# Kernel tuning notes

Hardware: AMD Instinct MI355X
Metric: run time of the kernel (lower is better)

Reference implementation:

```python
import jax, jax.numpy as jnp
import numpy as np

VOCAB = 50000
EMBED = 256
LABELS = 2
DEPTH = 10          # complete binary tree: 2**DEPTH leaves
B = 256             # batch of trees
L = 2 ** DEPTH      # leaves per tree


def setup_inputs() -> dict:
    key = jax.random.key(0)
    ks = jax.random.split(key, 7)
    token_ids = jax.random.randint(ks[0], (B, L), 0, VOCAB)
    labels = jax.random.randint(ks[1], (B,), 0, LABELS)
    emb = jax.random.normal(ks[2], (VOCAB, EMBED), dtype=jnp.float32)
    W_w = jax.random.normal(ks[3], (EMBED, 2 * EMBED), dtype=jnp.float32) * (1.0 / np.sqrt(2 * EMBED))
    W_b = jax.random.normal(ks[4], (EMBED,), dtype=jnp.float32) * 0.01
    P_w = jax.random.normal(ks[5], (LABELS, EMBED), dtype=jnp.float32) * (1.0 / np.sqrt(EMBED))
    P_b = jax.random.normal(ks[6], (LABELS,), dtype=jnp.float32) * 0.01
    return {"token_ids": token_ids, "labels": labels, "emb": emb,
            "W_w": W_w, "W_b": W_b, "P_w": P_w, "P_b": P_b}


def reference(token_ids, labels, emb, W_w, W_b, P_w, P_b):
    # Leaves: relu(embedding(token))  -> [B, L, E]
    x = jax.nn.relu(emb[token_ids])
    # Level-by-level combine: currentNode = relu(W @ cat(left, right) + b)
    # Leaf order is left-to-right, so adjacent pairs (2k, 2k+1) are siblings;
    # reshape concatenates (left, right) along features, matching torch.cat((l, r), 1).
    while x.shape[1] > 1:
        bsz, n, e = x.shape
        lr = x.reshape(bsz, n // 2, 2 * e)                       # [B, n/2, 2E]
        x = jax.nn.relu(jnp.einsum('bnf,ef->bne', lr, W_w) + W_b)
    root = x[:, 0]                                               # [B, E]
    logits = root @ P_w.T + P_b                                  # [B, label_size]
    prediction = jnp.argmax(logits, axis=1)
    logp = jax.nn.log_softmax(logits, axis=-1)
    loss = -jnp.take_along_axis(logp, labels[:, None], axis=1)[:, 0]  # per-tree CE
    return prediction, loss
```

## Files before the change

### kernel.cpp

```cpp
#include <hip/hip_runtime.h>
#include <hip/hip_bf16.h>
#include <math.h>

#define EMBED   256
#define KDIM    512
#define BATCH   256
#define BM      128
#define VOCAB   50000

typedef float  f32x4   __attribute__((ext_vector_type(4)));
typedef __bf16 bf16x8  __attribute__((ext_vector_type(8)));
typedef unsigned short ushort8 __attribute__((ext_vector_type(8)));

__device__ __forceinline__ unsigned short f2h(float f) {
    unsigned int u = __float_as_uint(f);
    u += 0x7FFFu + ((u >> 16) & 1u);
    return (unsigned short)(u >> 16);
}
__device__ __forceinline__ float h2f(unsigned short h) {
    return __uint_as_float(((unsigned int)h) << 16);
}
__device__ __forceinline__ void gload16(const void* g, void* l) {
    __builtin_amdgcn_global_load_lds(
        (const __attribute__((address_space(1))) unsigned int*)g,
        (__attribute__((address_space(3))) unsigned int*)l, 16, 0, 0);
}

__global__ __launch_bounds__(256) void prep_emb(const float* __restrict__ emb,
                                                unsigned short* __restrict__ Eh,
                                                unsigned short* __restrict__ El)
{
    const size_t base = ((size_t)blockIdx.x * 256 + threadIdx.x) * 8;
    float v[8];
    *(float4*)&v[0] = *(const float4*)&emb[base];
    *(float4*)&v[4] = *(const float4*)&emb[base + 4];
    ushort8 hs, ls;
    #pragma unroll
    for (int i = 0; i < 8; ++i) {
        const float f = fmaxf(v[i], 0.f);
        const unsigned short h = f2h(f);
        hs[i] = h;
        ls[i] = f2h(f - h2f(h));
    }
    *(ushort8*)&Eh[base] = hs;
    *(ushort8*)&El[base] = ls;
}

__global__ __launch_bounds__(256) void prep_w(const float* __restrict__ W,
                                              unsigned short* __restrict__ Wh,
                                              unsigned short* __restrict__ Wl)
{
    const int i = blockIdx.x * 256 + threadIdx.x;
    const float w = W[i];
    const unsigned short h = f2h(w);
    Wh[i] = h;
    Wl[i] = f2h(w - h2f(h));
}

template<int LV1, int WPREP>
__global__ __launch_bounds__(512) void gemm_tree(
    const unsigned short* __restrict__ Xh, const unsigned short* __restrict__ Xl,
    const unsigned short* __restrict__ Wh, const unsigned short* __restrict__ Wl,
    const float*  __restrict__ Wf,
    const float*  __restrict__ bias,
    unsigned short* __restrict__ Yh, unsigned short* __restrict__ Yl,
    const int* __restrict__ tok,
    const unsigned short* __restrict__ Eh, const unsigned short* __restrict__ El)
{
    __shared__ __align__(16) unsigned short AhL[4096], AlL[4096];
    __shared__ __align__(16) unsigned short BhL[8192], BlL[8192];

    const int tid = threadIdx.x;
    const int wid = tid >> 6;
    const int l   = tid & 63;
    const int q   = l >> 4;
    const int rr  = l & 15;
    const int m0  = blockIdx.x * BM;

    const int waveM = wid >> 2;
    const int waveN = wid & 3;

    int tk0 = 0, tk1 = 0;
    if constexpr (LV1) {
        const int r = m0 + wid * 16 + rr;
        tk0 = tok[2 * r];
        tk1 = tok[2 * r + 1];
    }

    f32x4 acc[4][4] = {};

    for (int t = 0; t < 16; ++t) {
        const int k0   = t << 5;
        const int joff = k0 >> 8;
        const int c    = (k0 & 255) + q * 8;

        if constexpr (LV1) {
            const size_t off = (size_t)(joff ? tk1 : tk0) * EMBED + c;
            gload16(Eh + off, &AhL[wid * 512]);
            gload16(El + off, &AlL[wid * 512]);
        } else {
            const size_t off = (size_t)(2 * (m0 + wid * 16 + rr) + joff) * EMBED + c;
            gload16(Xh + off, &AhL[wid * 512]);
            gload16(Xl + off, &AlL[wid * 512]);
        }

        #pragma unroll
        for (int g = 0; g < 2; ++g) {
            const int s = wid + g * 8;
            if constexpr (WPREP) {
                const size_t off = (size_t)(s * 16 + rr) * KDIM + k0 + q * 8;
                gload16(Wh + off, &BhL[s * 512]);
                gload16(Wl + off, &BlL[s * 512]);
            } else {
                const float* ws = Wf + (size_t)(s * 16 + rr) * KDIM + k0 + q * 8;
                float v[8];
                *(float4*)&v[0] = *(const float4*)ws;
                *(float4*)&v[4] = *(const float4*)(ws + 4);
                ushort8 hs, ls;
                #pragma unroll
                for (int i = 0; i < 8; ++i) {
                    const unsigned short h = f2h(v[i]);
                    hs[i] = h;
                    ls[i] = f2h(v[i] - h2f(h));
                }
                *(ushort8*)&BhL[s * 512 + l * 8] = hs;
                *(ushort8*)&BlL[s * 512 + l * 8] = ls;
            }
        }

        __syncthreads();

        bf16x8 ah[4], al[4], bh[4], bl[4];
        #pragma unroll
        for (int mi = 0; mi < 4; ++mi) {
            ah[mi] = *(const bf16x8*)&AhL[(waveM * 4 + mi) * 512 + l * 8];
            al[mi] = *(const bf16x8*)&AlL[(waveM * 4 + mi) * 512 + l * 8];
        }
        #pragma unroll
        for (int ni = 0; ni < 4; ++ni) {
            bh[ni] = *(const bf16x8*)&BhL[(waveN * 4 + ni) * 512 + l * 8];
            bl[ni] = *(const bf16x8*)&BlL[(waveN * 4 + ni) * 512 + l * 8];
        }
        #pragma unroll
        for (int mi = 0; mi < 4; ++mi)
            #pragma unroll
            for (int ni = 0; ni < 4; ++ni)
                acc[mi][ni] = __builtin_amdgcn_mfma_f32_16x16x32_bf16(ah[mi], bh[ni], acc[mi][ni], 0, 0, 0);
        #pragma unroll
        for (int mi = 0; mi < 4; ++mi)
            #pragma unroll
            for (int ni = 0; ni < 4; ++ni)
                acc[mi][ni] = __builtin_amdgcn_mfma_f32_16x16x32_bf16(al[mi], bh[ni], acc[mi][ni], 0, 0, 0);
        #pragma unroll
        for (int mi = 0; mi < 4; ++mi)
            #pragma unroll
            for (int ni = 0; ni < 4; ++ni)
                acc[mi][ni] = __builtin_amdgcn_mfma_f32_16x16x32_bf16(ah[mi], bl[ni], acc[mi][ni], 0, 0, 0);

        __syncthreads();
    }

    #pragma unroll
    for (int ni = 0; ni < 4; ++ni) {
        const int col = waveN * 64 + ni * 16 + rr;
        const float bv = bias[col];
        #pragma unroll
        for (int mi = 0; mi < 4; ++mi) {
            const int row0 = m0 + waveM * 64 + mi * 16 + q * 4;
            #pragma unroll
            for (int jj = 0; jj < 4; ++jj) {
                const float y = fmaxf(acc[mi][ni][jj] + bv, 0.f);
                const unsigned short h = f2h(y);
                Yh[(size_t)(row0 + jj) * EMBED + col] = h;
                Yl[(size_t)(row0 + jj) * EMBED + col] = f2h(y - h2f(h));
            }
        }
    }
}

template<int WPREP>
__global__ __launch_bounds__(256) void tail_kernel(
    const unsigned short* __restrict__ A4h, const unsigned short* __restrict__ A4l,
    const unsigned short* __restrict__ Wh, const unsigned short* __restrict__ Wl,
    const float* __restrict__ Wf, const float* __restrict__ bias,
    const float* __restrict__ Pw, const float* __restrict__ Pb,
    const int* __restrict__ labels, float* __restrict__ out)
{
    __shared__ __align__(16) unsigned short X0h[8192], X0l[8192];
    __shared__ __align__(16) unsigned short X1h[4096], X1l[4096];
    __shared__ __align__(16) unsigned short BhT[2][8192], BlT[2][8192];
    __shared__ __align__(16) unsigned short Asth[2][1024], Astl[2][1024];

    const int tid = threadIdx.x;
    const int w   = tid >> 6;
    const int l   = tid & 63;
    const int q   = l >> 4;
    const int rr  = l & 15;
    const int b   = blockIdx.x;

    auto stageB = [&](int buf, int k0) {
        if constexpr (WPREP) {
            #pragma unroll
            for (int j = 0; j < 8; ++j) {
                const int sb = w * 8 + j;
                const int s  = sb & 15;
                const size_t off = (size_t)(s * 16 + rr) * KDIM + k0 + q * 8;
                if (sb < 16) gload16(Wh + off, &BhT[buf][s * 512]);
                else         gload16(Wl + off, &BlT[buf][s * 512]);
            }
        } else {
            #pragma unroll
            for (int j = 0; j < 4; ++j) {
                const int u = w * 4 + j;
                const float* ws = Wf + (size_t)(u * 16 + rr) * KDIM + k0 + q * 8;
                float v[8];
                *(float4*)&v[0] = *(const float4*)ws;
                *(float4*)&v[4] = *(const float4*)(ws + 4);
                ushort8 hs, ls;
                #pragma unroll
                for (int i = 0; i < 8; ++i) {
                    const unsigned short h = f2h(v[i]);
                    hs[i] = h;
                    ls[i] = f2h(v[i] - h2f(h));
                }
                *(ushort8*)&BhT[buf][u * 512 + l * 8] = hs;
                *(ushort8*)&BlT[buf][u * 512 + l * 8] = ls;
            }
        }
    };

    auto stageA = [&](int buf, int t) {
        if (w < 2) {
            const int k0   = t * 32;
            const int joff = k0 >> 8;
            const int c    = (k0 & 255) + q * 8;
            const size_t off = (size_t)(64 * b + 2 * (w * 16 + rr) + joff) * EMBED + c;
            gload16(A4h + off, &Asth[buf][w * 512]);
            gload16(A4l + off, &Astl[buf][w * 512]);
        }
    };

    float bv[4];
    #pragma unroll
    for (int ni = 0; ni < 4; ++ni) bv[ni] = bias[w * 64 + ni * 16 + rr];

    stageB(0, 0);
    stageA(0, 0);
    __syncthreads();

    int g = 0;
    for (int s = 0; s < 6; ++s) {
        unsigned short* srch = (s & 1) ? X0h : X1h;
        unsigned short* srcl = (s & 1) ? X0l : X1l;
        unsigned short* dsth = (s & 1) ? X1h : X0h;
        unsigned short* dstl = (s & 1) ? X1l : X0l;
        const int Mout = 32 >> s;

        f32x4 acc[2][4] = {};
        for (int t = 0; t < 16; ++t, ++g) {
            const int cur = g & 1;
            if (g < 95) stageB(cur ^ 1, ((t + 1) & 15) * 32);
            if (s == 0 && t < 15) stageA(cur ^ 1, t + 1);

            const int k0   = t * 32;
            const int joff = k0 >> 8;
            const int c    = (k0 & 255) + q * 8;

            bf16x8 a_h0, a_l0;
            if (s == 0) {
                a_h0 = *(const bf16x8*)&Asth[cur][l * 8];
                a_l0 = *(const bf16x8*)&Astl[cur][l * 8];
            } else {
                const int row = 2 * rr + joff;
                const int idx = (row * 256 + c) ^ ((row & 7) << 3);
                a_h0 = *(const bf16x8*)&srch[idx];
                a_l0 = *(const bf16x8*)&srcl[idx];
            }

            bf16x8 bh4[4], bl4[4];
            #pragma unroll
            for (int ni = 0; ni < 4; ++ni) {
                bh4[ni] = *(const bf16x8*)&BhT[cur][(w * 4 + ni) * 512 + l * 8];
                bl4[ni] = *(const bf16x8*)&BlT[cur][(w * 4 + ni) * 512 + l * 8];
            }
            #pragma unroll
            for (int ni = 0; ni < 4; ++ni)
                acc[0][ni] = __builtin_amdgcn_mfma_f32_16x16x32_bf16(a_h0, bh4[ni], acc[0][ni], 0, 0, 0);
            #pragma unroll
            for (int ni = 0; ni < 4; ++ni)
                acc[0][ni] = __builtin_amdgcn_mfma_f32_16x16x32_bf16(a_l0, bh4[ni], acc[0][ni], 0, 0, 0);
            #pragma unroll
            for (int ni = 0; ni < 4; ++ni)
                acc[0][ni] = __builtin_amdgcn_mfma_f32_16x16x32_bf16(a_h0, bl4[ni], acc[0][ni], 0, 0, 0);

            if (s == 0) {
                const bf16x8 a_h1 = *(const bf16x8*)&Asth[cur][512 + l * 8];
                const bf16x8 a_l1 = *(const bf16x8*)&Astl[cur][512 + l * 8];
                #pragma unroll
                for (int ni = 0; ni < 4; ++ni)
                    acc[1][ni] = __builtin_amdgcn_mfma_f32_16x16x32_bf16(a_h1, bh4[ni], acc[1][ni], 0, 0, 0);
                #pragma unroll
                for (int ni = 0; ni < 4; ++ni)
                    acc[1][ni] = __builtin_amdgcn_mfma_f32_16x16x32_bf16(a_l1, bh4[ni], acc[1][ni], 0, 0, 0);
                #pragma unroll
                for (int ni = 0; ni < 4; ++ni)
                    acc[1][ni] = __builtin_amdgcn_mfma_f32_16x16x32_bf16(a_h1, bl4[ni], acc[1][ni], 0, 0, 0);
            }
            __syncthreads();
        }

        #pragma unroll
        for (int ni = 0; ni < 4; ++ni) {
            const int col = w * 64 + ni * 16 + rr;
            #pragma unroll
            for (int jj = 0; jj < 4; ++jj) {
                const int row = q * 4 + jj;
                if (row < Mout) {
                    const float y = fmaxf(acc[0][ni][jj] + bv[ni], 0.f);
                    const unsigned short h = f2h(y);
                    const int idx = (row * 256 + col) ^ ((row & 7) << 3);
                    dsth[idx] = h;
                    dstl[idx] = f2h(y - h2f(h));
                }
            }
            if (s == 0) {
                #pragma unroll
                for (int jj = 0; jj < 4; ++jj) {
                    const int row = 16 + q * 4 + jj;
                    const float y = fmaxf(acc[1][ni][jj] + bv[ni], 0.f);
                    const unsigned short h = f2h(y);
                    const int idx = (row * 256 + col) ^ ((row & 7) << 3);
                    dsth[idx] = h;
                    dstl[idx] = f2h(y - h2f(h));
                }
            }
        }
        __syncthreads();
    }

    if (w == 0) {
        float s0 = 0.f, s1 = 0.f;
        #pragma unroll
        for (int i = 0; i < 4; ++i) {
            const int col = l + i * 64;
            const float x = h2f(X1h[col]) + h2f(X1l[col]);
            s0 = fmaf(x, Pw[col], s0);
            s1 = fmaf(x, Pw[EMBED + col], s1);
        }
        #pragma unroll
        for (int off = 32; off > 0; off >>= 1) {
            s0 += __shfl_down(s0, off);
            s1 += __shfl_down(s1, off);
        }
        if (l == 0) {
            const float l0 = s0 + Pb[0];
            const float l1 = s1 + Pb[1];
            const int pred = (l1 > l0) ? 1 : 0;
            const float m  = fmaxf(l0, l1);
            const float lse = m + logf(expf(l0 - m) + expf(l1 - m));
            const int lab = labels[b];
            out[b]         = (float)pred;
            out[BATCH + b] = lse - (lab ? l1 : l0);
        }
    }
}

extern "C" void kernel_launch(void* const* d_in, const int* in_sizes, int n_in,
                              void* d_out, int out_size, void* d_ws, size_t ws_size,
                              hipStream_t stream)
{
    const int*   token_ids = (const int*)d_in[0];
    const int*   labels    = (const int*)d_in[1];
    const float* emb       = (const float*)d_in[2];
    const float* W_w       = (const float*)d_in[3];
    const float* W_b       = (const float*)d_in[4];
    const float* P_w       = (const float*)d_in[5];
    const float* P_b       = (const float*)d_in[6];
    float*       out       = (float*)d_out;

    unsigned short* Ah_buf = (unsigned short*)d_ws;
    unsigned short* Al_buf = Ah_buf + (size_t)131072 * 256;
    unsigned short* Bh_buf = Al_buf + (size_t)131072 * 256;
    unsigned short* Bl_buf = Bh_buf + (size_t)65536 * 256;
    unsigned short* Wh     = Bl_buf + (size_t)65536 * 256;
    unsigned short* Wl     = Wh + 131072;
    unsigned short* Eh     = Bh_buf;
    unsigned short* El     = Bl_buf;

    const size_t need_wprep = ((size_t)131072 * 256 * 2 + (size_t)65536 * 256 * 2 + 2 * 131072) * 2;
    const bool wprep = ws_size >= need_wprep;

    if (wprep) prep_w<<<512, 256, 0, stream>>>(W_w, Wh, Wl);
    prep_emb<<<(VOCAB * EMBED) / 2048, 256, 0, stream>>>(emb, Eh, El);

    if (wprep) {
        gemm_tree<1,1><<<1024, 512, 0, stream>>>(nullptr, nullptr, Wh, Wl, W_w, W_b, Ah_buf, Al_buf, token_ids, Eh, El);
        gemm_tree<0,1><<< 512, 512, 0, stream>>>(Ah_buf, Al_buf, Wh, Wl, W_w, W_b, Bh_buf, Bl_buf, nullptr, nullptr, nullptr);
        gemm_tree<0,1><<< 256, 512, 0, stream>>>(Bh_buf, Bl_buf, Wh, Wl, W_w, W_b, Ah_buf, Al_buf, nullptr, nullptr, nullptr);
        gemm_tree<0,1><<< 128, 512, 0, stream>>>(Ah_buf, Al_buf, Wh, Wl, W_w, W_b, Bh_buf, Bl_buf, nullptr, nullptr, nullptr);
        tail_kernel<1><<<BATCH, 256, 0, stream>>>(Bh_buf, Bl_buf, Wh, Wl, W_w, W_b, P_w, P_b, labels, out);
    } else {
        gemm_tree<1,0><<<1024, 512, 0, stream>>>(nullptr, nullptr, Wh, Wl, W_w, W_b, Ah_buf, Al_buf, token_ids, Eh, El);
        gemm_tree<0,0><<< 512, 512, 0, stream>>>(Ah_buf, Al_buf, Wh, Wl, W_w, W_b, Bh_buf, Bl_buf, nullptr, nullptr, nullptr);
        gemm_tree<0,0><<< 256, 512, 0, stream>>>(Bh_buf, Bl_buf, Wh, Wl, W_w, W_b, Ah_buf, Al_buf, nullptr, nullptr, nullptr);
        gemm_tree<0,0><<< 128, 512, 0, stream>>>(Ah_buf, Al_buf, Wh, Wl, W_w, W_b, Bh_buf, Bl_buf, nullptr, nullptr, nullptr);
        tail_kernel<0><<<BATCH, 256, 0, stream>>>(Bh_buf, Bl_buf, Wh, Wl, W_w, W_b, P_w, P_b, labels, out);
    }
}
```

Before: 452.0 us.

## Split GEMM tree tiles along N and merge prep kernels into one launch

Each gemm_tree block now computes a 128x128 output tile with 256 threads instead of a 128x256 tile with 512 threads. The N dimension is split across a second grid axis, which doubles the block count and halves LDS use per block, so occupancy and parallelism should rise, especially on the small later levels. The cost is that each A tile (embedding gather or previous-level activations) is loaded twice, once per N half. The embedding and weight split-prep kernels are also fused into a single launch to save one kernel launch.

```diff
diff --git a/kernel.cpp b/kernel.cpp
--- a/kernel.cpp
+++ b/kernel.cpp
@@ -26,39 +26,41 @@
         (__attribute__((address_space(3))) unsigned int*)l, 16, 0, 0);
 }
 
-__global__ __launch_bounds__(256) void prep_emb(const float* __restrict__ emb,
+__global__ __launch_bounds__(256) void prep_all(const float* __restrict__ emb,
                                                 unsigned short* __restrict__ Eh,
-                                                unsigned short* __restrict__ El)
+                                                unsigned short* __restrict__ El,
+                                                const float* __restrict__ W,
+                                                unsigned short* __restrict__ Wh,
+                                                unsigned short* __restrict__ Wl,
+                                                int wprep)
 {
-    const size_t base = ((size_t)blockIdx.x * 256 + threadIdx.x) * 8;
-    float v[8];
-    *(float4*)&v[0] = *(const float4*)&emb[base];
-    *(float4*)&v[4] = *(const float4*)&emb[base + 4];
-    ushort8 hs, ls;
-    #pragma unroll
-    for (int i = 0; i < 8; ++i) {
-        const float f = fmaxf(v[i], 0.f);
-        const unsigned short h = f2h(f);
-        hs[i] = h;
-        ls[i] = f2h(f - h2f(h));
-    }
-    *(ushort8*)&Eh[base] = hs;
-    *(ushort8*)&El[base] = ls;
-}
-
-__global__ __launch_bounds__(256) void prep_w(const float* __restrict__ W,
-                                              unsigned short* __restrict__ Wh,
-                                              unsigned short* __restrict__ Wl)
-{
-    const int i = blockIdx.x * 256 + threadIdx.x;
-    const float w = W[i];
-    const unsigned short h = f2h(w);
-    Wh[i] = h;
-    Wl[i] = f2h(w - h2f(h));
+    const int bid = blockIdx.x;
+    if (bid < 6250) {
+        const size_t base = ((size_t)bid * 256 + threadIdx.x) * 8;
+        float v[8];
+        *(float4*)&v[0] = *(const float4*)&emb[base];
+        *(float4*)&v[4] = *(const float4*)&emb[base + 4];
+        ushort8 hs, ls;
+        #pragma unroll
+        for (int i = 0; i < 8; ++i) {
+            const float f = fmaxf(v[i], 0.f);
+            const unsigned short h = f2h(f);
+            hs[i] = h;
+            ls[i] = f2h(f - h2f(h));
+        }
+        *(ushort8*)&Eh[base] = hs;
+        *(ushort8*)&El[base] = ls;
+    } else if (wprep) {
+        const int i = (bid - 6250) * 256 + threadIdx.x;
+        const float w = W[i];
+        const unsigned short h = f2h(w);
+        Wh[i] = h;
+        Wl[i] = f2h(w - h2f(h));
+    }
 }
 
 template<int LV1, int WPREP>
-__global__ __launch_bounds__(512) void gemm_tree(
+__global__ __launch_bounds__(256) void gemm_tree(
     const unsigned short* __restrict__ Xh, const unsigned short* __restrict__ Xl,
     const unsigned short* __restrict__ Wh, const unsigned short* __restrict__ Wl,
     const float*  __restrict__ Wf,
@@ -68,23 +70,27 @@
     const unsigned short* __restrict__ Eh, const unsigned short* __restrict__ El)
 {
     __shared__ __align__(16) unsigned short AhL[4096], AlL[4096];
-    __shared__ __align__(16) unsigned short BhL[8192], BlL[8192];
+    __shared__ __align__(16) unsigned short BhL[4096], BlL[4096];
 
     const int tid = threadIdx.x;
-    const int wid = tid >> 6;
+    const int w   = tid >> 6;
     const int l   = tid & 63;
     const int q   = l >> 4;
     const int rr  = l & 15;
-    const int m0  = blockIdx.x * BM;
-
-    const int waveM = wid >> 2;
-    const int waveN = wid & 3;
-
-    int tk0 = 0, tk1 = 0;
+    const int m0  = blockIdx.y * BM;
+    const int n0  = blockIdx.x * 128;
+
+    const int waveM = w >> 1;
+    const int waveN = w & 1;
+
+    int tk[2][2];
     if constexpr (LV1) {
-        const int r = m0 + wid * 16 + rr;
-        tk0 = tok[2 * r];
-        tk1 = tok[2 * r + 1];
+        #pragma unroll
+        for (int g = 0; g < 2; ++g) {
+            const int r = m0 + (w + g * 4) * 16 + rr;
+            tk[g][0] = tok[2 * r];
+            tk[g][1] = tok[2 * r + 1];
+        }
     }
 
     f32x4 acc[4][4] = {};
@@ -94,25 +100,25 @@
         const int joff = k0 >> 8;
         const int c    = (k0 & 255) + q * 8;
 
-        if constexpr (LV1) {
-            const size_t off = (size_t)(joff ? tk1 : tk0) * EMBED + c;
-            gload16(Eh + off, &AhL[wid * 512]);
-            gload16(El + off, &AlL[wid * 512]);
-        } else {
-            const size_t off = (size_t)(2 * (m0 + wid * 16 + rr) + joff) * EMBED + c;
-            gload16(Xh + off, &AhL[wid * 512]);
-            gload16(Xl + off, &AlL[wid * 512]);
-        }
-
         #pragma unroll
         for (int g = 0; g < 2; ++g) {
-            const int s = wid + g * 8;
+            const int s = w + g * 4;
+            if constexpr (LV1) {
+                const int  tkg = joff ? tk[g][1] : tk[g][0];
+                const size_t off = (size_t)tkg * EMBED + c;
+                gload16(Eh + off, &AhL[s * 512]);
+                gload16(El + off, &AlL[s * 512]);
+            } else {
+                const size_t off = (size_t)(2 * (m0 + s * 16 + rr) + joff) * EMBED + c;
+                gload16(Xh + off, &AhL[s * 512]);
+                gload16(Xl + off, &AlL[s * 512]);
+            }
             if constexpr (WPREP) {
-                const size_t off = (size_t)(s * 16 + rr) * KDIM + k0 + q * 8;
-                gload16(Wh + off, &BhL[s * 512]);
-                gload16(Wl + off, &BlL[s * 512]);
+                const size_t woff = (size_t)(n0 + s * 16 + rr) * KDIM + k0 + q * 8;
+                gload16(Wh + woff, &BhL[s * 512]);
+                gload16(Wl + woff, &BlL[s * 512]);
             } else {
-                const float* ws = Wf + (size_t)(s * 16 + rr) * KDIM + k0 + q * 8;
+                const float* ws = Wf + (size_t)(n0 + s * 16 + rr) * KDIM + k0 + q * 8;
                 float v[8];
                 *(float4*)&v[0] = *(const float4*)ws;
                 *(float4*)&v[4] = *(const float4*)(ws + 4);
@@ -162,7 +168,7 @@
 
     #pragma unroll
     for (int ni = 0; ni < 4; ++ni) {
-        const int col = waveN * 64 + ni * 16 + rr;
+        const int col = n0 + waveN * 64 + ni * 16 + rr;
         const float bv = bias[col];
         #pragma unroll
         for (int mi = 0; mi < 4; ++mi) {
@@ -390,20 +396,19 @@
     const size_t need_wprep = ((size_t)131072 * 256 * 2 + (size_t)65536 * 256 * 2 + 2 * 131072) * 2;
     const bool wprep = ws_size >= need_wprep;
 
-    if (wprep) prep_w<<<512, 256, 0, stream>>>(W_w, Wh, Wl);
-    prep_emb<<<(VOCAB * EMBED) / 2048, 256, 0, stream>>>(emb, Eh, El);
+    prep_all<<<6762, 256, 0, stream>>>(emb, Eh, El, W_w, Wh, Wl, wprep ? 1 : 0);
 
     if (wprep) {
-        gemm_tree<1,1><<<1024, 512, 0, stream>>>(nullptr, nullptr, Wh, Wl, W_w, W_b, Ah_buf, Al_buf, token_ids, Eh, El);
-        gemm_tree<0,1><<< 512, 512, 0, stream>>>(Ah_buf, Al_buf, Wh, Wl, W_w, W_b, Bh_buf, Bl_buf, nullptr, nullptr, nullptr);
-        gemm_tree<0,1><<< 256, 512, 0, stream>>>(Bh_buf, Bl_buf, Wh, Wl, W_w, W_b, Ah_buf, Al_buf, nullptr, nullptr, nullptr);
-        gemm_tree<0,1><<< 128, 512, 0, stream>>>(Ah_buf, Al_buf, Wh, Wl, W_w, W_b, Bh_buf, Bl_buf, nullptr, nullptr, nullptr);
+        gemm_tree<1,1><<<dim3(2,1024), 256, 0, stream>>>(nullptr, nullptr, Wh, Wl, W_w, W_b, Ah_buf, Al_buf, token_ids, Eh, El);
+        gemm_tree<0,1><<<dim3(2, 512), 256, 0, stream>>>(Ah_buf, Al_buf, Wh, Wl, W_w, W_b, Bh_buf, Bl_buf, nullptr, nullptr, nullptr);
+        gemm_tree<0,1><<<dim3(2, 256), 256, 0, stream>>>(Bh_buf, Bl_buf, Wh, Wl, W_w, W_b, Ah_buf, Al_buf, nullptr, nullptr, nullptr);
+        gemm_tree<0,1><<<dim3(2, 128), 256, 0, stream>>>(Ah_buf, Al_buf, Wh, Wl, W_w, W_b, Bh_buf, Bl_buf, nullptr, nullptr, nullptr);
         tail_kernel<1><<<BATCH, 256, 0, stream>>>(Bh_buf, Bl_buf, Wh, Wl, W_w, W_b, P_w, P_b, labels, out);
     } else {
-        gemm_tree<1,0><<<1024, 512, 0, stream>>>(nullptr, nullptr, Wh, Wl, W_w, W_b, Ah_buf, Al_buf, token_ids, Eh, El);
-        gemm_tree<0,0><<< 512, 512, 0, stream>>>(Ah_buf, Al_buf, Wh, Wl, W_w, W_b, Bh_buf, Bl_buf, nullptr, nullptr, nullptr);
-        gemm_tree<0,0><<< 256, 512, 0, stream>>>(Bh_buf, Bl_buf, Wh, Wl, W_w, W_b, Ah_buf, Al_buf, nullptr, nullptr, nullptr);
-        gemm_tree<0,0><<< 128, 512, 0, stream>>>(Ah_buf, Al_buf, Wh, Wl, W_w, W_b, Bh_buf, Bl_buf, nullptr, nullptr, nullptr);
+        gemm_tree<1,0><<<dim3(2,1024), 256, 0, stream>>>(nullptr, nullptr, Wh, Wl, W_w, W_b, Ah_buf, Al_buf, token_ids, Eh, El);
+        gemm_tree<0,0><<<dim3(2, 512), 256, 0, stream>>>(Ah_buf, Al_buf, Wh, Wl, W_w, W_b, Bh_buf, Bl_buf, nullptr, nullptr, nullptr);
+        gemm_tree<0,0><<<dim3(2, 256), 256, 0, stream>>>(Bh_buf, Bl_buf, Wh, Wl, W_w, W_b, Ah_buf, Al_buf, nullptr, nullptr, nullptr);
+        gemm_tree<0,0><<<dim3(2, 128), 256, 0, stream>>>(Ah_buf, Al_buf, Wh, Wl, W_w, W_b, Bh_buf, Bl_buf, nullptr, nullptr, nullptr);
         tail_kernel<0><<<BATCH, 256, 0, stream>>>(Bh_buf, Bl_buf, Wh, Wl, W_w, W_b, P_w, P_b, labels, out);
     }
 }
```

After: 457.4 us. About the same (+1.2%).

## Triple-buffer GEMM tree levels with async LDS loads and merge prep kernels

Applied to the files above, without the earlier changes.

Adds a gemm_pipe kernel that triple-buffers the A and B tiles in LDS, prefetching three K-steps ahead with direct global-to-LDS loads and fine-grained vmcnt waits. It replaces the single-buffered load/sync/compute loop on the default path, so global latency can overlap the MFMA work. The embedding and weight split-precision prep kernels are also merged into one launch to save launch overhead. Tripling LDS use (about 144 KB per block) limits occupancy to one block per CU, and the hand-placed waitcnt and barrier sequencing is fragile.

```diff
diff --git a/kernel.cpp b/kernel.cpp
--- a/kernel.cpp
+++ b/kernel.cpp
@@ -26,41 +26,170 @@
         (__attribute__((address_space(3))) unsigned int*)l, 16, 0, 0);
 }
 
-__global__ __launch_bounds__(256) void prep_emb(const float* __restrict__ emb,
+__global__ __launch_bounds__(256) void prep_all(const float* __restrict__ emb,
                                                 unsigned short* __restrict__ Eh,
-                                                unsigned short* __restrict__ El)
+                                                unsigned short* __restrict__ El,
+                                                const float* __restrict__ W,
+                                                unsigned short* __restrict__ Wh,
+                                                unsigned short* __restrict__ Wl,
+                                                int wprep)
 {
-    const size_t base = ((size_t)blockIdx.x * 256 + threadIdx.x) * 8;
-    float v[8];
-    *(float4*)&v[0] = *(const float4*)&emb[base];
-    *(float4*)&v[4] = *(const float4*)&emb[base + 4];
-    ushort8 hs, ls;
+    const int bid = blockIdx.x;
+    if (bid < 6250) {
+        const size_t base = ((size_t)bid * 256 + threadIdx.x) * 8;
+        float v[8];
+        *(float4*)&v[0] = *(const float4*)&emb[base];
+        *(float4*)&v[4] = *(const float4*)&emb[base + 4];
+        ushort8 hs, ls;
+        #pragma unroll
+        for (int i = 0; i < 8; ++i) {
+            const float f = fmaxf(v[i], 0.f);
+            const unsigned short h = f2h(f);
+            hs[i] = h;
+            ls[i] = f2h(f - h2f(h));
+        }
+        *(ushort8*)&Eh[base] = hs;
+        *(ushort8*)&El[base] = ls;
+    } else if (wprep) {
+        const int i = (bid - 6250) * 256 + threadIdx.x;
+        const float w = W[i];
+        const unsigned short h = f2h(w);
+        Wh[i] = h;
+        Wl[i] = f2h(w - h2f(h));
+    }
+}
+
+template<int LV1>
+__global__ __launch_bounds__(512) void gemm_pipe(
+    const unsigned short* __restrict__ Xh, const unsigned short* __restrict__ Xl,
+    const unsigned short* __restrict__ Wh, const unsigned short* __restrict__ Wl,
+    const float*  __restrict__ bias,
+    unsigned short* __restrict__ Yh, unsigned short* __restrict__ Yl,
+    const int* __restrict__ tok,
+    const unsigned short* __restrict__ Eh, const unsigned short* __restrict__ El)
+{
+    __shared__ __align__(16) unsigned short AhL[3][4096], AlL[3][4096];
+    __shared__ __align__(16) unsigned short BhL[3][8192], BlL[3][8192];
+
+    const int tid = threadIdx.x;
+    const int wid = tid >> 6;
+    const int l   = tid & 63;
+    const int q   = l >> 4;
+    const int rr  = l & 15;
+    const int m0  = blockIdx.x * BM;
+
+    const int waveM = wid >> 2;
+    const int waveN = wid & 3;
+
+    int tk0 = 0, tk1 = 0;
+    if constexpr (LV1) {
+        const int r = m0 + wid * 16 + rr;
+        tk0 = tok[2 * r];
+        tk1 = tok[2 * r + 1];
+    }
+
+    auto stage = [&](int buf, int t) {
+        const int k0   = t << 5;
+        const int joff = k0 >> 8;
+        const int c    = (k0 & 255) + q * 8;
+        if constexpr (LV1) {
+            const size_t off = (size_t)(joff ? tk1 : tk0) * EMBED + c;
+            gload16(Eh + off, &AhL[buf][wid * 512]);
+            gload16(El + off, &AlL[buf][wid * 512]);
+        } else {
+            const size_t off = (size_t)(2 * (m0 + wid * 16 + rr) + joff) * EMBED + c;
+            gload16(Xh + off, &AhL[buf][wid * 512]);
+            gload16(Xl + off, &AlL[buf][wid * 512]);
+        }
+        #pragma unroll
+        for (int g = 0; g < 2; ++g) {
+            const int s = wid + g * 8;
+            const size_t woff = (size_t)(s * 16 + rr) * KDIM + k0 + q * 8;
+            gload16(Wh + woff, &BhL[buf][s * 512]);
+            gload16(Wl + woff, &BlL[buf][s * 512]);
+        }
+    };
+
+    f32x4 acc[4][4] = {};
+
+    stage(0, 0);
+    stage(1, 1);
+    stage(2, 2);
+    asm volatile("s_waitcnt vmcnt(12)" ::: "memory");
+    __builtin_amdgcn_sched_barrier(0);
+    __builtin_amdgcn_s_barrier();
+    __builtin_amdgcn_sched_barrier(0);
+
+    int cur = 0;
+    for (int t = 0; t < 16; ++t) {
+        bf16x8 ah[4], al[4], bh[4], bl[4];
+        #pragma unroll
+        for (int mi = 0; mi < 4; ++mi) {
+            ah[mi] = *(const bf16x8*)&AhL[cur][(waveM * 4 + mi) * 512 + l * 8];
+            al[mi] = *(const bf16x8*)&AlL[cur][(waveM * 4 + mi) * 512 + l * 8];
+        }
+        #pragma unroll
+        for (int ni = 0; ni < 4; ++ni) {
+            bh[ni] = *(const bf16x8*)&BhL[cur][(waveN * 4 + ni) * 512 + l * 8];
+            bl[ni] = *(const bf16x8*)&BlL[cur][(waveN * 4 + ni) * 512 + l * 8];
+        }
+        asm volatile("s_waitcnt lgkmcnt(0)" ::: "memory");
+        __builtin_amdgcn_sched_barrier(0);
+        __builtin_amdgcn_s_barrier();
+        __builtin_amdgcn_sched_barrier(0);
+
+        if (t + 3 < 16) stage(cur, t + 3);
+
+        __builtin_amdgcn_s_setprio(1);
+        #pragma unroll
+        for (int mi = 0; mi < 4; ++mi)
+            #pragma unroll
+            for (int ni = 0; ni < 4; ++ni)
+                acc[mi][ni] = __builtin_amdgcn_mfma_f32_16x16x32_bf16(ah[mi], bh[ni], acc[mi][ni], 0, 0, 0);
+        #pragma unroll
+        for (int mi = 0; mi < 4; ++mi)
+            #pragma unroll
+            for (int ni = 0; ni < 4; ++ni)
+                acc[mi][ni] = __builtin_amdgcn_mfma_f32_16x16x32_bf16(al[mi], bh[ni], acc[mi][ni], 0, 0, 0);
+        #pragma unroll
+        for (int mi = 0; mi < 4; ++mi)
+            #pragma unroll
+            for (int ni = 0; ni < 4; ++ni)
+                acc[mi][ni] = __builtin_amdgcn_mfma_f32_16x16x32_bf16(ah[mi], bl[ni], acc[mi][ni], 0, 0, 0);
+        __builtin_amdgcn_s_setprio(0);
+
+        if (t < 15) {
+            if (t <= 12)      { asm volatile("s_waitcnt vmcnt(12)" ::: "memory"); }
+            else if (t == 13) { asm volatile("s_waitcnt vmcnt(6)"  ::: "memory"); }
+            else              { asm volatile("s_waitcnt vmcnt(0)"  ::: "memory"); }
+            __builtin_amdgcn_sched_barrier(0);
+            __builtin_amdgcn_s_barrier();
+            __builtin_amdgcn_sched_barrier(0);
+        }
+        cur = (cur == 2) ? 0 : cur + 1;
+    }
+
     #pragma unroll
-    for (int i = 0; i < 8; ++i) {
-        const float f = fmaxf(v[i], 0.f);
-        const unsigned short h = f2h(f);
-        hs[i] = h;
-        ls[i] = f2h(f - h2f(h));
-    }
-    *(ushort8*)&Eh[base] = hs;
-    *(ushort8*)&El[base] = ls;
-}
-
-__global__ __launch_bounds__(256) void prep_w(const float* __restrict__ W,
-                                              unsigned short* __restrict__ Wh,
-                                              unsigned short* __restrict__ Wl)
-{
-    const int i = blockIdx.x * 256 + threadIdx.x;
-    const float w = W[i];
-    const unsigned short h = f2h(w);
-    Wh[i] = h;
-    Wl[i] = f2h(w - h2f(h));
-}
-
-template<int LV1, int WPREP>
+    for (int ni = 0; ni < 4; ++ni) {
+        const int col = waveN * 64 + ni * 16 + rr;
+        const float bv = bias[col];
+        #pragma unroll
+        for (int mi = 0; mi < 4; ++mi) {
+            const int row0 = m0 + waveM * 64 + mi * 16 + q * 4;
+            #pragma unroll
+            for (int jj = 0; jj < 4; ++jj) {
+                const float y = fmaxf(acc[mi][ni][jj] + bv, 0.f);
+                const unsigned short h = f2h(y);
+                Yh[(size_t)(row0 + jj) * EMBED + col] = h;
+                Yl[(size_t)(row0 + jj) * EMBED + col] = f2h(y - h2f(h));
+            }
+        }
+    }
+}
+
+template<int LV1>
 __global__ __launch_bounds__(512) void gemm_tree(
     const unsigned short* __restrict__ Xh, const unsigned short* __restrict__ Xl,
-    const unsigned short* __restrict__ Wh, const unsigned short* __restrict__ Wl,
     const float*  __restrict__ Wf,
     const float*  __restrict__ bias,
     unsigned short* __restrict__ Yh, unsigned short* __restrict__ Yl,
@@ -76,7 +205,6 @@
     const int q   = l >> 4;
     const int rr  = l & 15;
     const int m0  = blockIdx.x * BM;
-
     const int waveM = wid >> 2;
     const int waveN = wid & 3;
 
@@ -103,31 +231,23 @@
             gload16(Xh + off, &AhL[wid * 512]);
             gload16(Xl + off, &AlL[wid * 512]);
         }
-
         #pragma unroll
         for (int g = 0; g < 2; ++g) {
             const int s = wid + g * 8;
-            if constexpr (WPREP) {
-                const size_t off = (size_t)(s * 16 + rr) * KDIM + k0 + q * 8;
-                gload16(Wh + off, &BhL[s * 512]);
-                gload16(Wl + off, &BlL[s * 512]);
-            } else {
-                const float* ws = Wf + (size_t)(s * 16 + rr) * KDIM + k0 + q * 8;
-                float v[8];
-                *(float4*)&v[0] = *(const float4*)ws;
-                *(float4*)&v[4] = *(const float4*)(ws + 4);
-                ushort8 hs, ls;
-                #pragma unroll
-                for (int i = 0; i < 8; ++i) {
-                    const unsigned short h = f2h(v[i]);
-                    hs[i] = h;
-                    ls[i] = f2h(v[i] - h2f(h));
-                }
-                *(ushort8*)&BhL[s * 512 + l * 8] = hs;
-                *(ushort8*)&BlL[s * 512 + l * 8] = ls;
-            }
-        }
-
+            const float* ws = Wf + (size_t)(s * 16 + rr) * KDIM + k0 + q * 8;
+            float v[8];
+            *(float4*)&v[0] = *(const float4*)ws;
+            *(float4*)&v[4] = *(const float4*)(ws + 4);
+            ushort8 hs, ls;
+            #pragma unroll
+            for (int i = 0; i < 8; ++i) {
+                const unsigned short h = f2h(v[i]);
+                hs[i] = h;
+                ls[i] = f2h(v[i] - h2f(h));
+            }
+            *(ushort8*)&BhL[s * 512 + l * 8] = hs;
+            *(ushort8*)&BlL[s * 512 + l * 8] = ls;
+        }
         __syncthreads();
 
         bf16x8 ah[4], al[4], bh[4], bl[4];
@@ -390,20 +510,19 @@
     const size_t need_wprep = ((size_t)131072 * 256 * 2 + (size_t)65536 * 256 * 2 + 2 * 131072) * 2;
     const bool wprep = ws_size >= need_wprep;
 
-    if (wprep) prep_w<<<512, 256, 0, stream>>>(W_w, Wh, Wl);
-    prep_emb<<<(VOCAB * EMBED) / 2048, 256, 0, stream>>>(emb, Eh, El);
+    prep_all<<<6762, 256, 0, stream>>>(emb, Eh, El, W_w, Wh, Wl, wprep ? 1 : 0);
 
     if (wprep) {
-        gemm_tree<1,1><<<1024, 512, 0, stream>>>(nullptr, nullptr, Wh, Wl, W_w, W_b, Ah_buf, Al_buf, token_ids, Eh, El);
-        gemm_tree<0,1><<< 512, 512, 0, stream>>>(Ah_buf, Al_buf, Wh, Wl, W_w, W_b, Bh_buf, Bl_buf, nullptr, nullptr, nullptr);
-        gemm_tree<0,1><<< 256, 512, 0, stream>>>(Bh_buf, Bl_buf, Wh, Wl, W_w, W_b, Ah_buf, Al_buf, nullptr, nullptr, nullptr);
-        gemm_tree<0,1><<< 128, 512, 0, stream>>>(Ah_buf, Al_buf, Wh, Wl, W_w, W_b, Bh_buf, Bl_buf, nullptr, nullptr, nullptr);
+        gemm_pipe<1><<<1024, 512, 0, stream>>>(nullptr, nullptr, Wh, Wl, W_b, Ah_buf, Al_buf, token_ids, Eh, El);
+        gemm_pipe<0><<< 512, 512, 0, stream>>>(Ah_buf, Al_buf, Wh, Wl, W_b, Bh_buf, Bl_buf, nullptr, nullptr, nullptr);
+        gemm_pipe<0><<< 256, 512, 0, stream>>>(Bh_buf, Bl_buf, Wh, Wl, W_b, Ah_buf, Al_buf, nullptr, nullptr, nullptr);
+        gemm_pipe<0><<< 128, 512, 0, stream>>>(Ah_buf, Al_buf, Wh, Wl, W_b, Bh_buf, Bl_buf, nullptr, nullptr, nullptr);
         tail_kernel<1><<<BATCH, 256, 0, stream>>>(Bh_buf, Bl_buf, Wh, Wl, W_w, W_b, P_w, P_b, labels, out);
     } else {
-        gemm_tree<1,0><<<1024, 512, 0, stream>>>(nullptr, nullptr, Wh, Wl, W_w, W_b, Ah_buf, Al_buf, token_ids, Eh, El);
-        gemm_tree<0,0><<< 512, 512, 0, stream>>>(Ah_buf, Al_buf, Wh, Wl, W_w, W_b, Bh_buf, Bl_buf, nullptr, nullptr, nullptr);
-        gemm_tree<0,0><<< 256, 512, 0, stream>>>(Bh_buf, Bl_buf, Wh, Wl, W_w, W_b, Ah_buf, Al_buf, nullptr, nullptr, nullptr);
-        gemm_tree<0,0><<< 128, 512, 0, stream>>>(Ah_buf, Al_buf, Wh, Wl, W_w, W_b, Bh_buf, Bl_buf, nullptr, nullptr, nullptr);
+        gemm_tree<1><<<1024, 512, 0, stream>>>(nullptr, nullptr, W_w, W_b, Ah_buf, Al_buf, token_ids, Eh, El);
+        gemm_tree<0><<< 512, 512, 0, stream>>>(Ah_buf, Al_buf, W_w, W_b, Bh_buf, Bl_buf, nullptr, nullptr, nullptr);
+        gemm_tree<0><<< 256, 512, 0, stream>>>(Bh_buf, Bl_buf, W_w, W_b, Ah_buf, Al_buf, nullptr, nullptr, nullptr);
+        gemm_tree<0><<< 128, 512, 0, stream>>>(Ah_buf, Al_buf, W_w, W_b, Bh_buf, Bl_buf, nullptr, nullptr, nullptr);
         tail_kernel<0><<<BATCH, 256, 0, stream>>>(Bh_buf, Bl_buf, Wh, Wl, W_w, W_b, P_w, P_b, labels, out);
     }
 }
```

Result: slower. 471.6 us (+4.3%).

## Fuse tree levels 3-5 into per-tree tail kernel and merge prep kernels

Applied to the files above, without the earlier changes.

Replaces the two small-grid gemm_tree launches for levels 3 and 4 with extra stages inside the per-tree tail kernel, which now does levels 3, 4 and 5 by staging through global scratch before continuing in LDS. The two prep kernels are also merged into a single launch. The aim is to cut launch overhead and the poorly-occupied 256- and 128-block GEMM launches. In exchange, the tail kernel runs only 256 blocks of 256 threads and does much more serial work per block, with larger LDS use and a big 8x4 accumulator tile, which may lower parallelism for level 3.

```diff
diff --git a/kernel.cpp b/kernel.cpp
--- a/kernel.cpp
+++ b/kernel.cpp
@@ -26,35 +26,39 @@
         (__attribute__((address_space(3))) unsigned int*)l, 16, 0, 0);
 }
 
-__global__ __launch_bounds__(256) void prep_emb(const float* __restrict__ emb,
+#define MFMA16(a,b,c) __builtin_amdgcn_mfma_f32_16x16x32_bf16((a),(b),(c),0,0,0)
+
+__global__ __launch_bounds__(256) void prep_all(const float* __restrict__ emb,
                                                 unsigned short* __restrict__ Eh,
-                                                unsigned short* __restrict__ El)
+                                                unsigned short* __restrict__ El,
+                                                const float* __restrict__ W,
+                                                unsigned short* __restrict__ Wh,
+                                                unsigned short* __restrict__ Wl,
+                                                int wprep)
 {
-    const size_t base = ((size_t)blockIdx.x * 256 + threadIdx.x) * 8;
-    float v[8];
-    *(float4*)&v[0] = *(const float4*)&emb[base];
-    *(float4*)&v[4] = *(const float4*)&emb[base + 4];
-    ushort8 hs, ls;
-    #pragma unroll
-    for (int i = 0; i < 8; ++i) {
-        const float f = fmaxf(v[i], 0.f);
-        const unsigned short h = f2h(f);
-        hs[i] = h;
-        ls[i] = f2h(f - h2f(h));
-    }
-    *(ushort8*)&Eh[base] = hs;
-    *(ushort8*)&El[base] = ls;
-}
-
-__global__ __launch_bounds__(256) void prep_w(const float* __restrict__ W,
-                                              unsigned short* __restrict__ Wh,
-                                              unsigned short* __restrict__ Wl)
-{
-    const int i = blockIdx.x * 256 + threadIdx.x;
-    const float w = W[i];
-    const unsigned short h = f2h(w);
-    Wh[i] = h;
-    Wl[i] = f2h(w - h2f(h));
+    const int bid = blockIdx.x;
+    if (bid < 6250) {
+        const size_t base = ((size_t)bid * 256 + threadIdx.x) * 8;
+        float v[8];
+        *(float4*)&v[0] = *(const float4*)&emb[base];
+        *(float4*)&v[4] = *(const float4*)&emb[base + 4];
+        ushort8 hs, ls;
+        #pragma unroll
+        for (int i = 0; i < 8; ++i) {
+            const float f = fmaxf(v[i], 0.f);
+            const unsigned short h = f2h(f);
+            hs[i] = h;
+            ls[i] = f2h(f - h2f(h));
+        }
+        *(ushort8*)&Eh[base] = hs;
+        *(ushort8*)&El[base] = ls;
+    } else if (wprep) {
+        const int i = (bid - 6250) * 256 + threadIdx.x;
+        const float w = W[i];
+        const unsigned short h = f2h(w);
+        Wh[i] = h;
+        Wl[i] = f2h(w - h2f(h));
+    }
 }
 
 template<int LV1, int WPREP>
@@ -103,7 +107,6 @@
             gload16(Xh + off, &AhL[wid * 512]);
             gload16(Xl + off, &AlL[wid * 512]);
         }
-
         #pragma unroll
         for (int g = 0; g < 2; ++g) {
             const int s = wid + g * 8;
@@ -145,17 +148,17 @@
         for (int mi = 0; mi < 4; ++mi)
             #pragma unroll
             for (int ni = 0; ni < 4; ++ni)
-                acc[mi][ni] = __builtin_amdgcn_mfma_f32_16x16x32_bf16(ah[mi], bh[ni], acc[mi][ni], 0, 0, 0);
+                acc[mi][ni] = MFMA16(ah[mi], bh[ni], acc[mi][ni]);
         #pragma unroll
         for (int mi = 0; mi < 4; ++mi)
             #pragma unroll
             for (int ni = 0; ni < 4; ++ni)
-                acc[mi][ni] = __builtin_amdgcn_mfma_f32_16x16x32_bf16(al[mi], bh[ni], acc[mi][ni], 0, 0, 0);
+                acc[mi][ni] = MFMA16(al[mi], bh[ni], acc[mi][ni]);
         #pragma unroll
         for (int mi = 0; mi < 4; ++mi)
             #pragma unroll
             for (int ni = 0; ni < 4; ++ni)
-                acc[mi][ni] = __builtin_amdgcn_mfma_f32_16x16x32_bf16(ah[mi], bl[ni], acc[mi][ni], 0, 0, 0);
+                acc[mi][ni] = MFMA16(ah[mi], bl[ni], acc[mi][ni]);
 
         __syncthreads();
     }
@@ -179,17 +182,18 @@
 }
 
 template<int WPREP>
-__global__ __launch_bounds__(256) void tail_kernel(
-    const unsigned short* __restrict__ A4h, const unsigned short* __restrict__ A4l,
+__global__ __launch_bounds__(256) void tail3(
+    const unsigned short* __restrict__ A2h, const unsigned short* __restrict__ A2l,
+    unsigned short* __restrict__ S3h, unsigned short* __restrict__ S3l,
     const unsigned short* __restrict__ Wh, const unsigned short* __restrict__ Wl,
     const float* __restrict__ Wf, const float* __restrict__ bias,
     const float* __restrict__ Pw, const float* __restrict__ Pb,
     const int* __restrict__ labels, float* __restrict__ out)
 {
+    __shared__ __align__(16) unsigned short BhT[2][8192], BlT[2][8192];
+    __shared__ __align__(16) unsigned short Asth[2][4096], Astl[2][4096];
     __shared__ __align__(16) unsigned short X0h[8192], X0l[8192];
     __shared__ __align__(16) unsigned short X1h[4096], X1l[4096];
-    __shared__ __align__(16) unsigned short BhT[2][8192], BlT[2][8192];
-    __shared__ __align__(16) unsigned short Asth[2][1024], Astl[2][1024];
 
     const int tid = threadIdx.x;
     const int w   = tid >> 6;
@@ -197,6 +201,9 @@
     const int q   = l >> 4;
     const int rr  = l & 15;
     const int b   = blockIdx.x;
+
+    unsigned short* L4h = S3h + (size_t)32768 * 256;
+    unsigned short* L4l = S3l + (size_t)32768 * 256;
 
     auto stageB = [&](int buf, int k0) {
         if constexpr (WPREP) {
@@ -229,53 +236,190 @@
         }
     };
 
-    auto stageA = [&](int buf, int t) {
-        if (w < 2) {
-            const int k0   = t * 32;
-            const int joff = k0 >> 8;
-            const int c    = (k0 & 255) + q * 8;
-            const size_t off = (size_t)(64 * b + 2 * (w * 16 + rr) + joff) * EMBED + c;
-            gload16(A4h + off, &Asth[buf][w * 512]);
-            gload16(A4l + off, &Astl[buf][w * 512]);
-        }
-    };
-
     float bv[4];
     #pragma unroll
     for (int ni = 0; ni < 4; ++ni) bv[ni] = bias[w * 64 + ni * 16 + rr];
 
+    int g = 0;
+
+    auto stageA3 = [&](int buf, int t) {
+        const int k0 = t * 32, joff = k0 >> 8, c = (k0 & 255) + q * 8;
+        #pragma unroll
+        for (int j = 0; j < 4; ++j) {
+            const int u = w * 4 + j, s = u & 7;
+            const size_t off = (size_t)(256 * b + 2 * (s * 16 + rr) + joff) * EMBED + c;
+            if (u < 8) gload16(A2h + off, &Asth[buf][s * 512]);
+            else       gload16(A2l + off, &Astl[buf][s * 512]);
+        }
+    };
     stageB(0, 0);
-    stageA(0, 0);
+    stageA3(0, 0);
     __syncthreads();
-
-    int g = 0;
-    for (int s = 0; s < 6; ++s) {
+    {
+        f32x4 acc[8][4] = {};
+        for (int t = 0; t < 16; ++t, ++g) {
+            const int cur = g & 1;
+            if (g < 127) stageB(cur ^ 1, ((t + 1) & 15) * 32);
+            if (t < 15)  stageA3((t + 1) & 1, t + 1);
+            bf16x8 bh4[4], bl4[4];
+            #pragma unroll
+            for (int ni = 0; ni < 4; ++ni) {
+                bh4[ni] = *(const bf16x8*)&BhT[cur][(w * 4 + ni) * 512 + l * 8];
+                bl4[ni] = *(const bf16x8*)&BlT[cur][(w * 4 + ni) * 512 + l * 8];
+            }
+            #pragma unroll
+            for (int mi = 0; mi < 8; ++mi) {
+                const bf16x8 a_h = *(const bf16x8*)&Asth[t & 1][mi * 512 + l * 8];
+                const bf16x8 a_l = *(const bf16x8*)&Astl[t & 1][mi * 512 + l * 8];
+                #pragma unroll
+                for (int ni = 0; ni < 4; ++ni) acc[mi][ni] = MFMA16(a_h, bh4[ni], acc[mi][ni]);
+                #pragma unroll
+                for (int ni = 0; ni < 4; ++ni) acc[mi][ni] = MFMA16(a_l, bh4[ni], acc[mi][ni]);
+                #pragma unroll
+                for (int ni = 0; ni < 4; ++ni) acc[mi][ni] = MFMA16(a_h, bl4[ni], acc[mi][ni]);
+            }
+            __syncthreads();
+        }
+        #pragma unroll
+        for (int ni = 0; ni < 4; ++ni) {
+            const int col = w * 64 + ni * 16 + rr;
+            #pragma unroll
+            for (int mi = 0; mi < 8; ++mi)
+                #pragma unroll
+                for (int jj = 0; jj < 4; ++jj) {
+                    const int row = mi * 16 + q * 4 + jj;
+                    const float y = fmaxf(acc[mi][ni][jj] + bv[ni], 0.f);
+                    const unsigned short h = f2h(y);
+                    S3h[(size_t)(128 * b + row) * EMBED + col] = h;
+                    S3l[(size_t)(128 * b + row) * EMBED + col] = f2h(y - h2f(h));
+                }
+        }
+    }
+    __syncthreads();
+
+    auto stageA4 = [&](int buf, int t) {
+        const int k0 = t * 32, joff = k0 >> 8, c = (k0 & 255) + q * 8;
+        #pragma unroll
+        for (int j = 0; j < 2; ++j) {
+            const int u = w * 2 + j, s = u & 3;
+            const size_t off = (size_t)(128 * b + 2 * (s * 16 + rr) + joff) * EMBED + c;
+            if (u < 4) gload16(S3h + off, &Asth[buf][s * 512]);
+            else       gload16(S3l + off, &Astl[buf][s * 512]);
+        }
+    };
+    stageA4(0, 0);
+    {
+        f32x4 acc[4][4] = {};
+        for (int t = 0; t < 16; ++t, ++g) {
+            const int cur = g & 1;
+            if (g < 127) stageB(cur ^ 1, ((t + 1) & 15) * 32);
+            if (t < 15)  stageA4((t + 1) & 1, t + 1);
+            bf16x8 bh4[4], bl4[4];
+            #pragma unroll
+            for (int ni = 0; ni < 4; ++ni) {
+                bh4[ni] = *(const bf16x8*)&BhT[cur][(w * 4 + ni) * 512 + l * 8];
+                bl4[ni] = *(const bf16x8*)&BlT[cur][(w * 4 + ni) * 512 + l * 8];
+            }
+            #pragma unroll
+            for (int mi = 0; mi < 4; ++mi) {
+                const bf16x8 a_h = *(const bf16x8*)&Asth[t & 1][mi * 512 + l * 8];
+                const bf16x8 a_l = *(const bf16x8*)&Astl[t & 1][mi * 512 + l * 8];
+                #pragma unroll
+                for (int ni = 0; ni < 4; ++ni) acc[mi][ni] = MFMA16(a_h, bh4[ni], acc[mi][ni]);
+                #pragma unroll
+                for (int ni = 0; ni < 4; ++ni) acc[mi][ni] = MFMA16(a_l, bh4[ni], acc[mi][ni]);
+                #pragma unroll
+                for (int ni = 0; ni < 4; ++ni) acc[mi][ni] = MFMA16(a_h, bl4[ni], acc[mi][ni]);
+            }
+            __syncthreads();
+        }
+        #pragma unroll
+        for (int ni = 0; ni < 4; ++ni) {
+            const int col = w * 64 + ni * 16 + rr;
+            #pragma unroll
+            for (int mi = 0; mi < 4; ++mi)
+                #pragma unroll
+                for (int jj = 0; jj < 4; ++jj) {
+                    const int row = mi * 16 + q * 4 + jj;
+                    const float y = fmaxf(acc[mi][ni][jj] + bv[ni], 0.f);
+                    const unsigned short h = f2h(y);
+                    L4h[(size_t)(64 * b + row) * EMBED + col] = h;
+                    L4l[(size_t)(64 * b + row) * EMBED + col] = f2h(y - h2f(h));
+                }
+        }
+    }
+    __syncthreads();
+
+    auto stageA5 = [&](int buf, int t) {
+        const int k0 = t * 32, joff = k0 >> 8, c = (k0 & 255) + q * 8;
+        const int u = w, s = u & 1;
+        const size_t off = (size_t)(64 * b + 2 * (s * 16 + rr) + joff) * EMBED + c;
+        if (u < 2) gload16(L4h + off, &Asth[buf][s * 512]);
+        else       gload16(L4l + off, &Astl[buf][s * 512]);
+    };
+    stageA5(0, 0);
+    {
+        f32x4 acc[2][4] = {};
+        for (int t = 0; t < 16; ++t, ++g) {
+            const int cur = g & 1;
+            if (g < 127) stageB(cur ^ 1, ((t + 1) & 15) * 32);
+            if (t < 15)  stageA5((t + 1) & 1, t + 1);
+            bf16x8 bh4[4], bl4[4];
+            #pragma unroll
+            for (int ni = 0; ni < 4; ++ni) {
+                bh4[ni] = *(const bf16x8*)&BhT[cur][(w * 4 + ni) * 512 + l * 8];
+                bl4[ni] = *(const bf16x8*)&BlT[cur][(w * 4 + ni) * 512 + l * 8];
+            }
+            #pragma unroll
+            for (int mi = 0; mi < 2; ++mi) {
+                const bf16x8 a_h = *(const bf16x8*)&Asth[t & 1][mi * 512 + l * 8];
+                const bf16x8 a_l = *(const bf16x8*)&Astl[t & 1][mi * 512 + l * 8];
+                #pragma unroll
+                for (int ni = 0; ni < 4; ++ni) acc[mi][ni] = MFMA16(a_h, bh4[ni], acc[mi][ni]);
+                #pragma unroll
+                for (int ni = 0; ni < 4; ++ni) acc[mi][ni] = MFMA16(a_l, bh4[ni], acc[mi][ni]);
+                #pragma unroll
+                for (int ni = 0; ni < 4; ++ni) acc[mi][ni] = MFMA16(a_h, bl4[ni], acc[mi][ni]);
+            }
+            __syncthreads();
+        }
+        #pragma unroll
+        for (int ni = 0; ni < 4; ++ni) {
+            const int col = w * 64 + ni * 16 + rr;
+            #pragma unroll
+            for (int mi = 0; mi < 2; ++mi)
+                #pragma unroll
+                for (int jj = 0; jj < 4; ++jj) {
+                    const int row = mi * 16 + q * 4 + jj;
+                    const float y = fmaxf(acc[mi][ni][jj] + bv[ni], 0.f);
+                    const unsigned short h = f2h(y);
+                    const int idx = (row * 256 + col) ^ ((row & 7) << 3);
+                    X0h[idx] = h;
+                    X0l[idx] = f2h(y - h2f(h));
+                }
+        }
+    }
+    __syncthreads();
+
+    for (int s = 1; s < 6; ++s) {
         unsigned short* srch = (s & 1) ? X0h : X1h;
         unsigned short* srcl = (s & 1) ? X0l : X1l;
         unsigned short* dsth = (s & 1) ? X1h : X0h;
         unsigned short* dstl = (s & 1) ? X1l : X0l;
         const int Mout = 32 >> s;
 
-        f32x4 acc[2][4] = {};
+        f32x4 acc[4] = {};
         for (int t = 0; t < 16; ++t, ++g) {
             const int cur = g & 1;
-            if (g < 95) stageB(cur ^ 1, ((t + 1) & 15) * 32);
-            if (s == 0 && t < 15) stageA(cur ^ 1, t + 1);
+            if (g < 127) stageB(cur ^ 1, ((t + 1) & 15) * 32);
 
             const int k0   = t * 32;
             const int joff = k0 >> 8;
             const int c    = (k0 & 255) + q * 8;
-
-            bf16x8 a_h0, a_l0;
-            if (s == 0) {
-                a_h0 = *(const bf16x8*)&Asth[cur][l * 8];
-                a_l0 = *(const bf16x8*)&Astl[cur][l * 8];
-            } else {
-                const int row = 2 * rr + joff;
-                const int idx = (row * 256 + c) ^ ((row & 7) << 3);
-                a_h0 = *(const bf16x8*)&srch[idx];
-                a_l0 = *(const bf16x8*)&srcl[idx];
-            }
+            const int row  = 2 * rr + joff;
+            const int idx  = (row * 256 + c) ^ ((row & 7) << 3);
+            const bf16x8 a_h = *(const bf16x8*)&srch[idx];
+            const bf16x8 a_l = *(const bf16x8*)&srcl[idx];
 
             bf16x8 bh4[4], bl4[4];
             #pragma unroll
@@ -284,28 +428,12 @@
                 bl4[ni] = *(const bf16x8*)&BlT[cur][(w * 4 + ni) * 512 + l * 8];
             }
             #pragma unroll
-            for (int ni = 0; ni < 4; ++ni)
-                acc[0][ni] = __builtin_amdgcn_mfma_f32_16x16x32_bf16(a_h0, bh4[ni], acc[0][ni], 0, 0, 0);
-            #pragma unroll
-            for (int ni = 0; ni < 4; ++ni)
-                acc[0][ni] = __builtin_amdgcn_mfma_f32_16x16x32_bf16(a_l0, bh4[ni], acc[0][ni], 0, 0, 0);
-            #pragma unroll
-            for (int ni = 0; ni < 4; ++ni)
-                acc[0][ni] = __builtin_amdgcn_mfma_f32_16x16x32_bf16(a_h0, bl4[ni], acc[0][ni], 0, 0, 0);
-
-            if (s == 0) {
-                const bf16x8 a_h1 = *(const bf16x8*)&Asth[cur][512 + l * 8];
-                const bf16x8 a_l1 = *(const bf16x8*)&Astl[cur][512 + l * 8];
-                #pragma unroll
-                for (int ni = 0; ni < 4; ++ni)
-                    acc[1][ni] = __builtin_amdgcn_mfma_f32_16x16x32_bf16(a_h1, bh4[ni], acc[1][ni], 0, 0, 0);
-                #pragma unroll
-                for (int ni = 0; ni < 4; ++ni)
-                    acc[1][ni] = __builtin_amdgcn_mfma_f32_16x16x32_bf16(a_l1, bh4[ni], acc[1][ni], 0, 0, 0);
-                #pragma unroll
-                for (int ni = 0; ni < 4; ++ni)
-                    acc[1][ni] = __builtin_amdgcn_mfma_f32_16x16x32_bf16(a_h1, bl4[ni], acc[1][ni], 0, 0, 0);
-            }
+            for (int ni = 0; ni < 4; ++ni) acc[ni] = MFMA16(a_h, bh4[ni], acc[ni]);
+            #pragma unroll
+            for (int ni = 0; ni < 4; ++ni) acc[ni] = MFMA16(a_l, bh4[ni], acc[ni]);
+            #pragma unroll
+            for (int ni = 0; ni < 4; ++ni) acc[ni] = MFMA16(a_h, bl4[ni], acc[ni]);
+
             __syncthreads();
         }
 
@@ -316,18 +444,7 @@
             for (int jj = 0; jj < 4; ++jj) {
                 const int row = q * 4 + jj;
                 if (row < Mout) {
-                    const float y = fmaxf(acc[0][ni][jj] + bv[ni], 0.f);
-                    const unsigned short h = f2h(y);
-                    const int idx = (row * 256 + col) ^ ((row & 7) << 3);
-                    dsth[idx] = h;
-                    dstl[idx] = f2h(y - h2f(h));
-                }
-            }
-            if (s == 0) {
-                #pragma unroll
-                for (int jj = 0; jj < 4; ++jj) {
-                    const int row = 16 + q * 4 + jj;
-                    const float y = fmaxf(acc[1][ni][jj] + bv[ni], 0.f);
+                    const float y = fmaxf(acc[ni][jj] + bv[ni], 0.f);
                     const unsigned short h = f2h(y);
                     const int idx = (row * 256 + col) ^ ((row & 7) << 3);
                     dsth[idx] = h;
@@ -390,20 +507,15 @@
     const size_t need_wprep = ((size_t)131072 * 256 * 2 + (size_t)65536 * 256 * 2 + 2 * 131072) * 2;
     const bool wprep = ws_size >= need_wprep;
 
-    if (wprep) prep_w<<<512, 256, 0, stream>>>(W_w, Wh, Wl);
-    prep_emb<<<(VOCAB * EMBED) / 2048, 256, 0, stream>>>(emb, Eh, El);
+    prep_all<<<6762, 256, 0, stream>>>(emb, Eh, El, W_w, Wh, Wl, wprep ? 1 : 0);
 
     if (wprep) {
         gemm_tree<1,1><<<1024, 512, 0, stream>>>(nullptr, nullptr, Wh, Wl, W_w, W_b, Ah_buf, Al_buf, token_ids, Eh, El);
         gemm_tree<0,1><<< 512, 512, 0, stream>>>(Ah_buf, Al_buf, Wh, Wl, W_w, W_b, Bh_buf, Bl_buf, nullptr, nullptr, nullptr);
-        gemm_tree<0,1><<< 256, 512, 0, stream>>>(Bh_buf, Bl_buf, Wh, Wl, W_w, W_b, Ah_buf, Al_buf, nullptr, nullptr, nullptr);
-        gemm_tree<0,1><<< 128, 512, 0, stream>>>(Ah_buf, Al_buf, Wh, Wl, W_w, W_b, Bh_buf, Bl_buf, nullptr, nullptr, nullptr);
-        tail_kernel<1><<<BATCH, 256, 0, stream>>>(Bh_buf, Bl_buf, Wh, Wl, W_w, W_b, P_w, P_b, labels, out);
+        tail3<1><<<BATCH, 256, 0, stream>>>(Bh_buf, Bl_buf, Ah_buf, Al_buf, Wh, Wl, W_w, W_b, P_w, P_b, labels, out);
     } else {
         gemm_tree<1,0><<<1024, 512, 0, stream>>>(nullptr, nullptr, Wh, Wl, W_w, W_b, Ah_buf, Al_buf, token_ids, Eh, El);
         gemm_tree<0,0><<< 512, 512, 0, stream>>>(Ah_buf, Al_buf, Wh, Wl, W_w, W_b, Bh_buf, Bl_buf, nullptr, nullptr, nullptr);
-        gemm_tree<0,0><<< 256, 512, 0, stream>>>(Bh_buf, Bl_buf, Wh, Wl, W_w, W_b, Ah_buf, Al_buf, nullptr, nullptr, nullptr);
-        gemm_tree<0,0><<< 128, 512, 0, stream>>>(Ah_buf, Al_buf, Wh, Wl, W_w, W_b, Bh_buf, Bl_buf, nullptr, nullptr, nullptr);
-        tail_kernel<0><<<BATCH, 256, 0, stream>>>(Bh_buf, Bl_buf, Wh, Wl, W_w, W_b, P_w, P_b, labels, out);
-    }
-}
+        tail3<0><<<BATCH, 256, 0, stream>>>(Bh_buf, Bl_buf, Ah_buf, Al_buf, Wh, Wl, W_w, W_b, P_w, P_b, labels, out);
+    }
+}
```

After: 409.6 us. 9.4% less time.
